# Kernel optimization log

Measured on AMD Instinct MI355X. Metric: run time of the kernel, lower is better.

The kernel has to match this reference:

```python
import jax, jax.numpy as jnp
import numpy as np
import math

MARGIN = 0.3
SCALE = 30.0
NUM_CLASSES = 100000
EMB_DIM = 512
BATCH = 1024


def setup_inputs() -> dict:
    key = jax.random.key(0)
    k1, k2, k3 = jax.random.split(key, 3)
    embeddings = jax.random.normal(k1, (BATCH, EMB_DIM), dtype=jnp.float32)
    labels = jax.random.randint(k2, (BATCH,), 0, NUM_CLASSES, dtype=jnp.int64)
    # xavier_uniform for weight [num_classes, embedding_dim]
    limit = math.sqrt(6.0 / (NUM_CLASSES + EMB_DIM))
    weight = jax.random.uniform(k3, (NUM_CLASSES, EMB_DIM), dtype=jnp.float32,
                                minval=-limit, maxval=limit)
    return {"embeddings": embeddings, "labels": labels, "weight": weight}


def reference(embeddings, labels, weight):
    cos_m = math.cos(MARGIN)
    sin_m = math.sin(MARGIN)
    th = math.cos(math.pi - MARGIN)
    mm = math.sin(math.pi - MARGIN) * MARGIN

    # normalize weight rows only (embeddings are NOT normalized in the original)
    w_norm = weight / jnp.linalg.norm(weight, axis=1, keepdims=True)
    cosine = jnp.einsum('bd,cd->bc', embeddings, w_norm)  # [B, C]
    sine = jnp.sqrt(jnp.clip(1.0 - cosine * cosine, 0.0, 1.0))
    phi = cosine * cos_m - sine * sin_m
    phi = jnp.where(cosine > th, phi, cosine - mm)

    one_hot = jax.nn.one_hot(labels, cosine.shape[1], dtype=cosine.dtype)
    logits = SCALE * (one_hot * phi + (1.0 - one_hot) * cosine)

    logp = jax.nn.log_softmax(logits, axis=-1)
    nll = -jnp.take_along_axis(logp, labels[:, None], axis=1)[:, 0]
    return jnp.mean(nll)
```

## Files before the change

### kernel.cpp

```cpp
#include <hip/hip_runtime.h>
#include <math.h>

#define B_N 1024
#define D_K 512
#define C_N 100000
#define SCALEF 30.0f
#define COS_M 0.9553364891256061f
#define SIN_M 0.29552020666133955f
#define TH_C (-0.9553364891256061f)
#define MM_C 0.08865606199840186f
#define FIXM 160.0f

#define BM 128
#define BN 128
#define NCT ((C_N + BN - 1) / BN)
#define NCTP 784

typedef short bf16x8 __attribute__((ext_vector_type(8)));
typedef float f32x4  __attribute__((ext_vector_type(4)));

__device__ inline unsigned bf16rne(float f) {
    unsigned u = __float_as_uint(f);
    u += 0x7fffu + ((u >> 16) & 1u);
    return u >> 16;
}
__device__ inline unsigned pk2(float lo, float hi) {
    return bf16rne(lo) | (bf16rne(hi) << 16);
}

__device__ static __forceinline__ void async16(const void* g, void* l) {
    __builtin_amdgcn_global_load_lds(
        (const __attribute__((address_space(1))) unsigned int*)g,
        (__attribute__((address_space(3))) unsigned int*)l, 16, 0, 0);
}

__global__ __launch_bounds__(256) void wcvt_kernel(const float* __restrict__ w,
                                                   unsigned short* __restrict__ wbf) {
    int wave = threadIdx.x >> 6;
    int lane = threadIdx.x & 63;
    int c = blockIdx.x * 4 + wave;
    if (c >= C_N) return;
    const float4* p = (const float4*)(w + (size_t)c * D_K);
    float4 a = p[lane];
    float4 b = p[lane + 64];
    float s = a.x*a.x + a.y*a.y + a.z*a.z + a.w*a.w
            + b.x*b.x + b.y*b.y + b.z*b.z + b.w*b.w;
    #pragma unroll
    for (int off = 32; off; off >>= 1) s += __shfl_xor(s, off, 64);
    float rn = 1.0f / sqrtf(s);
    uint2 o0, o1;
    o0.x = pk2(a.x * rn, a.y * rn); o0.y = pk2(a.z * rn, a.w * rn);
    o1.x = pk2(b.x * rn, b.y * rn); o1.y = pk2(b.z * rn, b.w * rn);
    uint2* q = (uint2*)(wbf + (size_t)c * D_K);
    q[lane] = o0;
    q[lane + 64] = o1;
}

__global__ __launch_bounds__(256) void embcvt_kernel(const float* __restrict__ e,
                                                     unsigned short* __restrict__ ebf) {
    int i = blockIdx.x * 256 + threadIdx.x;
    float4 v = ((const float4*)e)[i];
    uint2 o;
    o.x = pk2(v.x, v.y);
    o.y = pk2(v.z, v.w);
    ((uint2*)ebf)[i] = o;
}

__global__ __launch_bounds__(256) void gemm_lse_kernel(
    const unsigned short* __restrict__ ebf, const unsigned short* __restrict__ wbf,
    const int* __restrict__ labels,
    float* __restrict__ partial, float* __restrict__ target)
{
    __shared__ short As[BM * 32];
    __shared__ short Bs[BN * 32];
    __shared__ int   labS[BM];
    __shared__ float sS[BM][2];

    const int bid = blockIdx.x;
    const int g = bid >> 6, r = (bid >> 3) & 7, j = bid & 7;
    const int ct = g * 8 + j;
    const int rt = r;
    const int row0 = rt * BM;
    const int col0 = ct * BN;
    const int t = threadIdx.x;
    const int lane = t & 63, wave = t >> 6;
    const int wx = wave & 1, wy = wave >> 1;
    const int lc = lane & 15, q = lane >> 4;

    if (t < BM) labS[t] = labels[row0 + t];
    __syncthreads();

    const int srow = t >> 2, skc = (t & 3) * 8;
    const unsigned short* aptr = ebf + (size_t)(row0 + srow) * D_K + skc;
    int brow0 = col0 + srow;        if (brow0 >= C_N) brow0 = C_N - 1;
    int brow1 = col0 + 64 + srow;   if (brow1 >= C_N) brow1 = C_N - 1;
    const unsigned short* bptr0 = wbf + (size_t)brow0 * D_K + skc;
    const unsigned short* bptr1 = wbf + (size_t)brow1 * D_K + skc;
    short* ldsA0 = As + t * 8;
    short* ldsA1 = As + t * 8 + 2048;
    short* ldsB0 = Bs + t * 8;
    short* ldsB1 = Bs + t * 8 + 2048;

    f32x4 acc[4][4] = {};

    for (int it = 0; it < D_K / 32; ++it) {
        const int k0 = it * 32;
        __syncthreads();
        async16(aptr + k0, ldsA0);
        async16(aptr + 64 * D_K + k0, ldsA1);
        async16(bptr0 + k0, ldsB0);
        async16(bptr1 + k0, ldsB1);
        __syncthreads();

        bf16x8 aF[4], bF[4];
        #pragma unroll
        for (int si = 0; si < 4; ++si)
            aF[si] = *(const bf16x8*)(As + (wy * 64 + si * 16 + lc) * 32 + q * 8);
        #pragma unroll
        for (int sj = 0; sj < 4; ++sj)
            bF[sj] = *(const bf16x8*)(Bs + (wx * 64 + sj * 16 + lc) * 32 + q * 8);
        #pragma unroll
        for (int si = 0; si < 4; ++si)
            #pragma unroll
            for (int sj = 0; sj < 4; ++sj)
                acc[si][sj] = __builtin_amdgcn_mfma_f32_16x16x32_bf16(
                    aF[si], bF[sj], acc[si][sj], 0, 0, 0);
    }

    #pragma unroll
    for (int si = 0; si < 4; ++si) {
        #pragma unroll
        for (int reg = 0; reg < 4; ++reg) {
            int rl = wy * 64 + si * 16 + q * 4 + reg;
            int lab = labS[rl];
            float s = 0.0f;
            #pragma unroll
            for (int sj = 0; sj < 4; ++sj) {
                int cg = col0 + wx * 64 + sj * 16 + lc;
                float cosv = acc[si][sj][reg];
                float v;
                if (cg == lab) {
                    float sine = sqrtf(fminf(fmaxf(1.0f - cosv * cosv, 0.0f), 1.0f));
                    float phi = cosv * COS_M - sine * SIN_M;
                    phi = (cosv > TH_C) ? phi : (cosv - MM_C);
                    v = SCALEF * phi;
                    target[row0 + rl] = v;
                } else {
                    v = SCALEF * cosv;
                }
                if (cg < C_N) s += __expf(v - FIXM);
            }
            #pragma unroll
            for (int off = 1; off < 16; off <<= 1)
                s += __shfl_xor(s, off, 64);
            if (lc == 0) sS[rl][wx] = s;
        }
    }
    __syncthreads();
    if (t < BM && ct < NCT)
        partial[(size_t)(row0 + t) * NCT + ct] = sS[t][0] + sS[t][1];
}

__global__ __launch_bounds__(256) void lse_reduce_kernel(
    const float* __restrict__ partial, const float* __restrict__ target,
    float* __restrict__ nll)
{
    int b = blockIdx.x;
    int t = threadIdx.x;
    float s = 0.0f;
    for (int ct = t; ct < NCT; ct += 256) s += partial[(size_t)b * NCT + ct];
    #pragma unroll
    for (int off = 1; off < 64; off <<= 1) s += __shfl_xor(s, off, 64);
    __shared__ float ss[4];
    int wave = t >> 6, lane = t & 63;
    if (lane == 0) ss[wave] = s;
    __syncthreads();
    if (t == 0) {
        s = ss[0] + ss[1] + ss[2] + ss[3];
        nll[b] = (FIXM + logf(s)) - target[b];
    }
}

__global__ __launch_bounds__(1024) void mean_kernel(const float* __restrict__ nll,
                                                    float* __restrict__ out) {
    int t = threadIdx.x;
    float v = nll[t];
    #pragma unroll
    for (int off = 1; off < 64; off <<= 1) v += __shfl_xor(v, off, 64);
    __shared__ float ws[16];
    int wave = t >> 6, lane = t & 63;
    if (lane == 0) ws[wave] = v;
    __syncthreads();
    if (t == 0) {
        float sum = 0.f;
        for (int w = 0; w < 16; ++w) sum += ws[w];
        out[0] = sum / (float)B_N;
    }
}

__global__ __launch_bounds__(256) void rnorm_fb_kernel(const float* __restrict__ w,
                                                       float* __restrict__ rnorm) {
    int wave = threadIdx.x >> 6;
    int lane = threadIdx.x & 63;
    int c = blockIdx.x * 4 + wave;
    if (c >= C_N) return;
    const float4* p = (const float4*)(w + (size_t)c * D_K);
    float4 a = p[lane];
    float4 b = p[lane + 64];
    float s = a.x*a.x + a.y*a.y + a.z*a.z + a.w*a.w
            + b.x*b.x + b.y*b.y + b.z*b.z + b.w*b.w;
    #pragma unroll
    for (int off = 32; off; off >>= 1) s += __shfl_xor(s, off, 64);
    if (lane == 0) rnorm[c] = 1.0f / sqrtf(s);
}

__device__ inline void merge_ms(float& m, float& s, float m2, float s2) {
    float M = fmaxf(m, m2);
    if (M != -INFINITY) {
        s = s * __expf(m - M) + s2 * __expf(m2 - M);
        m = M;
    }
}

#define ROWS 40
__global__ __launch_bounds__(256) void gemm_lse_fb_kernel(
    const unsigned short* __restrict__ ebf, const float* __restrict__ wgt,
    const int* __restrict__ labels, const float* __restrict__ rnorm,
    float2* __restrict__ partial, float* __restrict__ target)
{
    __shared__ short As[BM * ROWS];
    __shared__ short Bs[BN * ROWS];
    __shared__ float rnS[BN];
    __shared__ int   labS[BM];
    __shared__ float2 msS[BM][2];

    const int rt = blockIdx.x;
    const int ct = blockIdx.y;
    const int row0 = rt * BM;
    const int col0 = ct * BN;
    const int t = threadIdx.x;
    const int lane = t & 63, wave = t >> 6;
    const int wx = wave & 1, wy = wave >> 1;
    const int lc = lane & 15, q = lane >> 4;

    if (t < BN) {
        int c = col0 + t;
        rnS[t] = (c < C_N) ? rnorm[c] : 0.0f;
    } else {
        labS[t - BN] = labels[row0 + (t - BN)];
    }
    __syncthreads();

    const int sr = t >> 1;
    const int sh = t & 1;
    const int cB = col0 + sr;
    const bool bval = cB < C_N;
    const float rn = rnS[sr];
    const unsigned short* aptr = ebf + (size_t)(row0 + sr) * D_K + sh * 16;
    const float* bptr0 = wgt + (size_t)(bval ? cB : 0) * D_K + sh * 16;

    f32x4 acc[4][4] = {};

    for (int it = 0; it < D_K / 32; ++it) {
        const int k0 = it * 32;
        uint4 a0 = ((const uint4*)(aptr + k0))[0];
        uint4 a1 = ((const uint4*)(aptr + k0))[1];
        float4 b0 = make_float4(0.f,0.f,0.f,0.f), b1 = b0, b2 = b0, b3 = b0;
        if (bval) {
            const float4* bp = (const float4*)(bptr0 + k0);
            b0 = bp[0]; b1 = bp[1]; b2 = bp[2]; b3 = bp[3];
        }
        uint4 w0, w1;
        w0.x = pk2(b0.x * rn, b0.y * rn); w0.y = pk2(b0.z * rn, b0.w * rn);
        w0.z = pk2(b1.x * rn, b1.y * rn); w0.w = pk2(b1.z * rn, b1.w * rn);
        w1.x = pk2(b2.x * rn, b2.y * rn); w1.y = pk2(b2.z * rn, b2.w * rn);
        w1.z = pk2(b3.x * rn, b3.y * rn); w1.w = pk2(b3.z * rn, b3.w * rn);

        __syncthreads();
        *(uint4*)(As + sr * ROWS + sh * 16)     = a0;
        *(uint4*)(As + sr * ROWS + sh * 16 + 8) = a1;
        *(uint4*)(Bs + sr * ROWS + sh * 16)     = w0;
        *(uint4*)(Bs + sr * ROWS + sh * 16 + 8) = w1;
        __syncthreads();

        bf16x8 aF[4], bF[4];
        #pragma unroll
        for (int si = 0; si < 4; ++si)
            aF[si] = *(const bf16x8*)(As + (wy * 64 + si * 16 + lc) * ROWS + q * 8);
        #pragma unroll
        for (int sj = 0; sj < 4; ++sj)
            bF[sj] = *(const bf16x8*)(Bs + (wx * 64 + sj * 16 + lc) * ROWS + q * 8);
        #pragma unroll
        for (int si = 0; si < 4; ++si)
            #pragma unroll
            for (int sj = 0; sj < 4; ++sj)
                acc[si][sj] = __builtin_amdgcn_mfma_f32_16x16x32_bf16(
                    aF[si], bF[sj], acc[si][sj], 0, 0, 0);
    }

    #pragma unroll
    for (int si = 0; si < 4; ++si) {
        #pragma unroll
        for (int reg = 0; reg < 4; ++reg) {
            int rl = wy * 64 + si * 16 + q * 4 + reg;
            int lab = labS[rl];
            float lg[4];
            float mx = -INFINITY;
            #pragma unroll
            for (int sj = 0; sj < 4; ++sj) {
                int cg = col0 + wx * 64 + sj * 16 + lc;
                float cosv = acc[si][sj][reg];
                float v;
                if (cg == lab) {
                    float sine = sqrtf(fminf(fmaxf(1.0f - cosv * cosv, 0.0f), 1.0f));
                    float phi = cosv * COS_M - sine * SIN_M;
                    phi = (cosv > TH_C) ? phi : (cosv - MM_C);
                    v = SCALEF * phi;
                    target[row0 + rl] = v;
                } else {
                    v = SCALEF * cosv;
                }
                if (cg >= C_N) v = -INFINITY;
                lg[sj] = v;
                mx = fmaxf(mx, v);
            }
            #pragma unroll
            for (int off = 1; off < 16; off <<= 1)
                mx = fmaxf(mx, __shfl_xor(mx, off, 64));
            float s = 0.0f;
            #pragma unroll
            for (int sj = 0; sj < 4; ++sj)
                if (lg[sj] != -INFINITY) s += __expf(lg[sj] - mx);
            #pragma unroll
            for (int off = 1; off < 16; off <<= 1)
                s += __shfl_xor(s, off, 64);
            if (lc == 0) msS[rl][wx] = make_float2(mx, s);
        }
    }
    __syncthreads();
    if (t < BM) {
        float2 p0 = msS[t][0], p1 = msS[t][1];
        float m = p0.x, s = p0.y;
        float M = fmaxf(m, p1.x);
        if (M != -INFINITY) {
            s = s * __expf(m - M) + p1.y * __expf(p1.x - M);
            m = M;
        }
        partial[(size_t)(row0 + t) * NCT + ct] = make_float2(m, s);
    }
}

__global__ __launch_bounds__(256) void lse_reduce_fb_kernel(
    const float2* __restrict__ partial, const float* __restrict__ target,
    float* __restrict__ nll)
{
    int b = blockIdx.x;
    int t = threadIdx.x;
    float m = -INFINITY, s = 0.0f;
    for (int ct = t; ct < NCT; ct += 256) {
        float2 p = partial[(size_t)b * NCT + ct];
        merge_ms(m, s, p.x, p.y);
    }
    #pragma unroll
    for (int off = 1; off < 64; off <<= 1) {
        float m2 = __shfl_xor(m, off, 64);
        float s2 = __shfl_xor(s, off, 64);
        merge_ms(m, s, m2, s2);
    }
    __shared__ float ms[4], ss[4];
    int wave = t >> 6, lane = t & 63;
    if (lane == 0) { ms[wave] = m; ss[wave] = s; }
    __syncthreads();
    if (t == 0) {
        m = ms[0]; s = ss[0];
        for (int w = 1; w < 4; ++w) merge_ms(m, s, ms[w], ss[w]);
        nll[b] = (m + logf(s)) - target[b];
    }
}

extern "C" void kernel_launch(void* const* d_in, const int* in_sizes, int n_in,
                              void* d_out, int out_size, void* d_ws, size_t ws_size,
                              hipStream_t stream) {
    const float* emb    = (const float*)d_in[0];
    const int*   labels = (const int*)d_in[1];
    const float* wgt    = (const float*)d_in[2];
    float* out = (float*)d_out;
    char* ws = (char*)d_ws;

    if (ws_size >= 106659840ull) {
        float* target        = (float*)(ws);
        float* nll           = (float*)(ws + 4096);
        float* partial       = (float*)(ws + 8192);
        unsigned short* ebf  = (unsigned short*)(ws + 3211264);
        unsigned short* wbf  = (unsigned short*)(ws + 4259840);

        wcvt_kernel<<<C_N / 4, 256, 0, stream>>>(wgt, wbf);
        embcvt_kernel<<<(B_N * D_K / 4) / 256, 256, 0, stream>>>(emb, ebf);
        gemm_lse_kernel<<<(NCTP / 8) * 64, 256, 0, stream>>>(ebf, wbf, labels, partial, target);
        lse_reduce_kernel<<<B_N, 256, 0, stream>>>(partial, target, nll);
        mean_kernel<<<1, 1024, 0, stream>>>(nll, out);
    } else {
        float*  rnorm   = (float*)(ws);
        float*  target  = (float*)(ws + 400000);
        float*  nll     = (float*)(ws + 404096);
        float2* partial = (float2*)(ws + 408192);
        unsigned short* ebf = (unsigned short*)(ws + 6814336);

        rnorm_fb_kernel<<<C_N / 4, 256, 0, stream>>>(wgt, rnorm);
        embcvt_kernel<<<(B_N * D_K / 4) / 256, 256, 0, stream>>>(emb, ebf);
        dim3 gridB(B_N / BM, NCT);
        gemm_lse_fb_kernel<<<gridB, 256, 0, stream>>>(ebf, wgt, labels, rnorm, partial, target);
        lse_reduce_fb_kernel<<<B_N, 256, 0, stream>>>(partial, target, nll);
        mean_kernel<<<1, 1024, 0, stream>>>(nll, out);
    }
}
```

Before: 455.1 us.

## Double GEMM K-tile with XOR-swizzled LDS and transpose partial-sum layout

The GEMM K-step grows from 32 to 64, which halves the number of barrier pairs per tile and doubles the async loads issued per iteration. LDS rows use an XOR-style slot rotation to avoid bank conflicts on the fragment reads. The per-tile partial sums are now stored column-tile-major, so the LSE reduce kernel reads them coalesced. That reduce kernel now has each thread own one row and uses only 8 blocks, which may cut its parallelism.

```diff
diff --git a/kernel.cpp b/kernel.cpp
--- a/kernel.cpp
+++ b/kernel.cpp
@@ -13,6 +13,7 @@
 
 #define BM 128
 #define BN 128
+#define BK 64
 #define NCT ((C_N + BN - 1) / BN)
 #define NCTP 784
 
@@ -71,15 +72,15 @@
     const int* __restrict__ labels,
     float* __restrict__ partial, float* __restrict__ target)
 {
-    __shared__ short As[BM * 32];
-    __shared__ short Bs[BN * 32];
+    __shared__ short As[BM * BK];
+    __shared__ short Bs[BN * BK];
     __shared__ int   labS[BM];
     __shared__ float sS[BM][2];
 
     const int bid = blockIdx.x;
-    const int g = bid >> 6, r = (bid >> 3) & 7, j = bid & 7;
-    const int ct = g * 8 + j;
-    const int rt = r;
+    const int g8 = bid >> 6, r8 = (bid >> 3) & 7, j8 = bid & 7;
+    const int ct = g8 * 8 + j8;
+    const int rt = r8;
     const int row0 = rt * BM;
     const int col0 = ct * BN;
     const int t = threadIdx.x;
@@ -90,41 +91,57 @@
     if (t < BM) labS[t] = labels[row0 + t];
     __syncthreads();
 
-    const int srow = t >> 2, skc = (t & 3) * 8;
-    const unsigned short* aptr = ebf + (size_t)(row0 + srow) * D_K + skc;
-    int brow0 = col0 + srow;        if (brow0 >= C_N) brow0 = C_N - 1;
-    int brow1 = col0 + 64 + srow;   if (brow1 >= C_N) brow1 = C_N - 1;
-    const unsigned short* bptr0 = wbf + (size_t)brow0 * D_K + skc;
-    const unsigned short* bptr1 = wbf + (size_t)brow1 * D_K + skc;
-    short* ldsA0 = As + t * 8;
-    short* ldsA1 = As + t * 8 + 2048;
-    short* ldsB0 = Bs + t * 8;
-    short* ldsB1 = Bs + t * 8 + 2048;
+    const int srow = t >> 3;
+    const int sslot = t & 7;
+    const int gch = (sslot - srow) & 7;
+    const unsigned short* aptr = ebf + (size_t)(row0 + srow) * D_K + gch * 8;
+    int bR[4];
+    #pragma unroll
+    for (int p = 0; p < 4; ++p) {
+        int br = col0 + 32 * p + srow;
+        bR[p] = (br < C_N) ? br : (C_N - 1);
+    }
+    const unsigned short* bptr[4] = {
+        wbf + (size_t)bR[0] * D_K + gch * 8, wbf + (size_t)bR[1] * D_K + gch * 8,
+        wbf + (size_t)bR[2] * D_K + gch * 8, wbf + (size_t)bR[3] * D_K + gch * 8 };
+    short* ldsA = As + t * 8;
+    short* ldsB = Bs + t * 8;
 
     f32x4 acc[4][4] = {};
 
-    for (int it = 0; it < D_K / 32; ++it) {
-        const int k0 = it * 32;
+    for (int it = 0; it < D_K / BK; ++it) {
+        const int k0 = it * BK;
         __syncthreads();
-        async16(aptr + k0, ldsA0);
-        async16(aptr + 64 * D_K + k0, ldsA1);
-        async16(bptr0 + k0, ldsB0);
-        async16(bptr1 + k0, ldsB1);
+        #pragma unroll
+        for (int p = 0; p < 4; ++p)
+            async16(aptr + (size_t)32 * p * D_K + k0, ldsA + p * 2048);
+        #pragma unroll
+        for (int p = 0; p < 4; ++p)
+            async16(bptr[p] + k0, ldsB + p * 2048);
         __syncthreads();
 
-        bf16x8 aF[4], bF[4];
-        #pragma unroll
-        for (int si = 0; si < 4; ++si)
-            aF[si] = *(const bf16x8*)(As + (wy * 64 + si * 16 + lc) * 32 + q * 8);
-        #pragma unroll
-        for (int sj = 0; sj < 4; ++sj)
-            bF[sj] = *(const bf16x8*)(Bs + (wx * 64 + sj * 16 + lc) * 32 + q * 8);
-        #pragma unroll
-        for (int si = 0; si < 4; ++si)
-            #pragma unroll
-            for (int sj = 0; sj < 4; ++sj)
-                acc[si][sj] = __builtin_amdgcn_mfma_f32_16x16x32_bf16(
-                    aF[si], bF[sj], acc[si][sj], 0, 0, 0);
+        #pragma unroll
+        for (int kh = 0; kh < 2; ++kh) {
+            bf16x8 aF[4], bF[4];
+            #pragma unroll
+            for (int si = 0; si < 4; ++si) {
+                int r = wy * 64 + si * 16 + lc;
+                int slot = (kh * 4 + q + r) & 7;
+                aF[si] = *(const bf16x8*)(As + r * BK + slot * 8);
+            }
+            #pragma unroll
+            for (int sj = 0; sj < 4; ++sj) {
+                int r = wx * 64 + sj * 16 + lc;
+                int slot = (kh * 4 + q + r) & 7;
+                bF[sj] = *(const bf16x8*)(Bs + r * BK + slot * 8);
+            }
+            #pragma unroll
+            for (int si = 0; si < 4; ++si)
+                #pragma unroll
+                for (int sj = 0; sj < 4; ++sj)
+                    acc[si][sj] = __builtin_amdgcn_mfma_f32_16x16x32_bf16(
+                        aF[si], bF[sj], acc[si][sj], 0, 0, 0);
+        }
     }
 
     #pragma unroll
@@ -158,26 +175,25 @@
     }
     __syncthreads();
     if (t < BM && ct < NCT)
-        partial[(size_t)(row0 + t) * NCT + ct] = sS[t][0] + sS[t][1];
+        partial[(size_t)ct * B_N + row0 + t] = sS[t][0] + sS[t][1];
 }
 
 __global__ __launch_bounds__(256) void lse_reduce_kernel(
     const float* __restrict__ partial, const float* __restrict__ target,
     float* __restrict__ nll)
 {
-    int b = blockIdx.x;
-    int t = threadIdx.x;
+    __shared__ float sS[2][128];
+    int b0 = blockIdx.x * 128;
+    int tb = threadIdx.x & 127;
+    int tc = threadIdx.x >> 7;
     float s = 0.0f;
-    for (int ct = t; ct < NCT; ct += 256) s += partial[(size_t)b * NCT + ct];
-    #pragma unroll
-    for (int off = 1; off < 64; off <<= 1) s += __shfl_xor(s, off, 64);
-    __shared__ float ss[4];
-    int wave = t >> 6, lane = t & 63;
-    if (lane == 0) ss[wave] = s;
-    __syncthreads();
-    if (t == 0) {
-        s = ss[0] + ss[1] + ss[2] + ss[3];
-        nll[b] = (FIXM + logf(s)) - target[b];
+    for (int ct = tc; ct < NCT; ct += 2)
+        s += partial[(size_t)ct * B_N + b0 + tb];
+    sS[tc][tb] = s;
+    __syncthreads();
+    if (threadIdx.x < 128) {
+        float tot = sS[0][tb] + sS[1][tb];
+        nll[b0 + tb] = (FIXM + logf(tot)) - target[b0 + tb];
     }
 }
 
@@ -397,7 +413,7 @@
         wcvt_kernel<<<C_N / 4, 256, 0, stream>>>(wgt, wbf);
         embcvt_kernel<<<(B_N * D_K / 4) / 256, 256, 0, stream>>>(emb, ebf);
         gemm_lse_kernel<<<(NCTP / 8) * 64, 256, 0, stream>>>(ebf, wbf, labels, partial, target);
-        lse_reduce_kernel<<<B_N, 256, 0, stream>>>(partial, target, nll);
+        lse_reduce_kernel<<<B_N / 128, 256, 0, stream>>>(partial, target, nll);
         mean_kernel<<<1, 1024, 0, stream>>>(nll, out);
     } else {
         float*  rnorm   = (float*)(ws);
```

Measured after the change: 536.1 us. +17.8%, slower.
